# Kernel optimization log

Hardware: AMD Instinct MI355X
Metric: run time of the kernel (lower is better)

The kernel has to match this reference:

```python
import jax, jax.numpy as jnp
import numpy as np

NQ, NS, D, C = 4096, 16384, 128, 64  # queries, support, embed dim, num classes
T = 1.0
INF = 1000.0


def setup_inputs() -> dict:
    key = jax.random.key(0)
    k1, k2, k3 = jax.random.split(key, 3)
    xs = jax.random.normal(k1, (NS, D), dtype=jnp.float32)
    xq = jax.random.normal(k2, (NQ, D), dtype=jnp.float32)
    # labels 0..C-1, every class present with equal counts (NS/C = 256 > 1)
    ys = jax.random.permutation(k3, jnp.arange(NS, dtype=jnp.int32) % C)
    pos = jnp.arange(NQ, dtype=jnp.int32)   # queries are the first NQ support rows
    yq = ys[pos]
    return {"xq": xq, "yq": yq, "xs": xs, "ys": ys, "pos": pos}


def reference(xq, yq, xs, ys, pos):
    # classes = sorted unique labels; with labels in [0, C) and all present,
    # torch.unique(ys) == arange(C), so class index of label y is y itself.
    classes = jnp.arange(C, dtype=ys.dtype)
    one_hot = (ys[:, None] == classes[None, :]).astype(xq.dtype)   # [NS, C]
    counts = one_hot.sum(axis=0)                                   # [C]
    yq_new = ys[pos]                                               # class idx of each query
    idx = counts[yq] > 1                                           # queries with >1 same-class support

    # leave-one-out class prototypes per query
    mus = one_hot.T @ xs                                           # [C, D] per-class sums
    M = mus[yq_new] - xq                                           # [NQ, D]
    denom = jnp.clip(counts[yq_new] - 1.0, 0.1, None)              # [NQ]
    proto = M / denom[:, None]
    # pos_logit uses unsquared L2 distance (cdist p=2 .diag()) in the source
    pos_logit = -jnp.sqrt(jnp.maximum(jnp.sum((xq - proto) ** 2, axis=-1), 0.0))  # [NQ]

    # l2_dist logits: -0.5 * ||xq_i - xs_j||^2 / T, via the GEMM expansion
    sq = (jnp.sum(xq * xq, -1)[:, None] + jnp.sum(xs * xs, -1)[None, :]
          - 2.0 * (xq @ xs.T))                                     # [NQ, NS]
    logit = -0.5 * jnp.maximum(sq, 0.0) / T

    ind = jnp.arange(NQ)
    logit = logit.at[ind, pos].set(0.0)                            # logit[ind, pos] *= 0
    logit = logit.at[ind, pos].add(jnp.where(idx, -INF, 0.0))      # -= INF where idx

    # per-class masked segment sum == logit @ one_hot  -> [NQ, C]
    summed = logit @ one_hot
    normalized = summed / (counts - 1.0)[None, :]
    neg_logit = jax.scipy.special.logsumexp(normalized, axis=1)    # [NQ]
    return jnp.mean(neg_logit - pos_logit)
```

## Files before the change

### kernel.cpp

```cpp
#include <hip/hip_runtime.h>
#include <hip/hip_bf16.h>

#define NQ 4096
#define NS 16384
#define DIM 128
#define NC 64
#define INFV 1000.0f

using bf16 = __hip_bfloat16;
typedef __attribute__((ext_vector_type(8))) short frag_ab;
typedef __attribute__((ext_vector_type(4))) float frag_cd;

__device__ inline frag_ab pack8(float4 a, float4 b) {
    union { __hip_bfloat16 h; short s; } u;
    frag_ab f;
    u.h = __float2bfloat16(a.x); f[0] = u.s;
    u.h = __float2bfloat16(a.y); f[1] = u.s;
    u.h = __float2bfloat16(a.z); f[2] = u.s;
    u.h = __float2bfloat16(a.w); f[3] = u.s;
    u.h = __float2bfloat16(b.x); f[4] = u.s;
    u.h = __float2bfloat16(b.y); f[5] = u.s;
    u.h = __float2bfloat16(b.z); f[6] = u.s;
    u.h = __float2bfloat16(b.w); f[7] = u.s;
    return f;
}

__global__ __launch_bounds__(128) void k1_stats(
    const float* __restrict__ xs, const int* __restrict__ ys,
    float* __restrict__ mus_p, float* __restrict__ csum_p,
    int* __restrict__ counts_p) {
    const int c = blockIdx.x >> 1, half = blockIdx.x & 1;
    const int w = threadIdx.x >> 6, lane = threadIdx.x & 63;
    const int s = half * 2 + w;
    const int base = s * (NS / 4);
    const float2* xs2 = (const float2*)xs;

    float2 macc = {0.f, 0.f};
    float sacc = 0.f;
    int cnt = 0;
    for (int i = 0; i < NS / 4; i += 64) {
        int y = ys[base + i + lane];
        unsigned long long m = __ballot(y == c);
        cnt += (int)__popcll(m);
        while (m) {
            int b = __ffsll((long long)m) - 1;
            m &= m - 1;
            int row = base + i + b;
            float2 v = xs2[(size_t)row * 64 + lane];
            macc.x += v.x; macc.y += v.y;
            sacc += v.x * v.x + v.y * v.y;
        }
    }
    ((float2*)mus_p)[(size_t)(c * 4 + s) * 64 + lane] = macc;
#pragma unroll
    for (int mm = 1; mm < 64; mm <<= 1) sacc += __shfl_xor(sacc, mm, 64);
    if (lane == 0) {
        csum_p[c * 4 + s] = sacc;
        counts_p[c * 4 + s] = cnt;
    }
}

__global__ __launch_bounds__(256) void k2_main(
    const float* __restrict__ xq, const int* __restrict__ yq,
    const float* __restrict__ xs, const int* __restrict__ ys,
    const int* __restrict__ pos,
    const float* __restrict__ mus_p, const float* __restrict__ csum_p,
    const int* __restrict__ counts_p, float* __restrict__ out) {
    __shared__ float mus_lds[64 * 132];
    __shared__ float cnt_lds[64];
    __shared__ float csum_lds[64];
    __shared__ float sqq_a[64], corr_a[64], pospl_a[64];
    __shared__ int cp_a[64];
    __shared__ float red[4];

    const int tid = threadIdx.x, w = tid >> 6, lane = tid & 63;
    const int quad = lane >> 4, l15 = lane & 15;
    const int qbase = blockIdx.x * 64 + w * 16;

#pragma unroll 4
    for (int r = 0; r < 32; ++r) {
        int i = r * 256 + tid;
        int c = i >> 7, d = i & 127;
        float ssum = 0.f;
#pragma unroll
        for (int s = 0; s < 4; ++s) ssum += mus_p[(size_t)(c * 4 + s) * 128 + d];
        mus_lds[c * 132 + d] = ssum;
    }
    if (tid < 64) {
        float cs = 0.f; int cc = 0;
#pragma unroll
        for (int s = 0; s < 4; ++s) { cs += csum_p[tid * 4 + s]; cc += counts_p[tid * 4 + s]; }
        csum_lds[tid] = cs;
        cnt_lds[tid] = (float)cc;
    }
    __syncthreads();

    {
        int q_loc = lane >> 2, chunk = lane & 3;
        int q = qbase + q_loc;
        int pi = pos[q];
        int yqi = yq[q];
        int cp = ys[pi];
        float cnt_p = cnt_lds[cp];
        float inv_d = 1.f / fmaxf(cnt_p - 1.f, 0.1f);
        bool idxq = cnt_lds[yqi] > 1.f;
        float sqq = 0.f, dotv = 0.f, sqs = 0.f, dd = 0.f;
#pragma unroll
        for (int t = 0; t < 8; ++t) {
            int d0 = chunk * 32 + t * 4;
            float4 a = *(const float4*)(xq + (size_t)q * DIM + d0);
            float4 b = *(const float4*)(xs + (size_t)pi * DIM + d0);
            float4 m = *(const float4*)(&mus_lds[cp * 132 + d0]);
            sqq += a.x * a.x + a.y * a.y + a.z * a.z + a.w * a.w;
            dotv += a.x * b.x + a.y * b.y + a.z * b.z + a.w * b.w;
            sqs += b.x * b.x + b.y * b.y + b.z * b.z + b.w * b.w;
            float ex;
            ex = a.x - (m.x - a.x) * inv_d; dd += ex * ex;
            ex = a.y - (m.y - a.y) * inv_d; dd += ex * ex;
            ex = a.z - (m.z - a.z) * inv_d; dd += ex * ex;
            ex = a.w - (m.w - a.w) * inv_d; dd += ex * ex;
        }
#pragma unroll
        for (int mm = 1; mm < 4; mm <<= 1) {
            sqq += __shfl_xor(sqq, mm, 64);
            dotv += __shfl_xor(dotv, mm, 64);
            sqs += __shfl_xor(sqs, mm, 64);
            dd += __shfl_xor(dd, mm, 64);
        }
        if (chunk == 0) {
            float raw = -0.5f * fmaxf(sqq + sqs - 2.f * dotv, 0.f);
            sqq_a[w * 16 + q_loc] = sqq;
            corr_a[w * 16 + q_loc] = (idxq ? -INFV : 0.f) - raw;
            pospl_a[w * 16 + q_loc] = -sqrtf(fmaxf(dd, 0.f));
            cp_a[w * 16 + q_loc] = cp;
        }
    }
    __syncthreads();

    frag_ab afr[4];
    {
        const float* src0 = xq + (size_t)(qbase + l15) * DIM + quad * 8;
#pragma unroll
        for (int kk = 0; kk < 4; ++kk) {
            const float* s = src0 + kk * 32;
            afr[kk] = pack8(*(const float4*)s, *(const float4*)(s + 4));
        }
    }
    frag_cd acc[4];
#pragma unroll
    for (int ct = 0; ct < 4; ++ct) {
#pragma unroll
        for (int e = 0; e < 4; ++e) acc[ct][e] = 0.f;
        const float* bsrc = &mus_lds[(ct * 16 + l15) * 132 + quad * 8];
        frag_ab bfr[4];
#pragma unroll
        for (int kk = 0; kk < 4; ++kk) {
            const float* s = bsrc + kk * 32;
            bfr[kk] = pack8(*(const float4*)s, *(const float4*)(s + 4));
        }
#pragma unroll
        for (int kk = 0; kk < 4; ++kk)
            acc[ct] = __builtin_amdgcn_mfma_f32_16x16x32_bf16(afr[kk], bfr[kk], acc[ct], 0, 0, 0);
    }

    float norm[4][4];
#pragma unroll
    for (int ct = 0; ct < 4; ++ct) {
        int cB = ct * 16 + l15;
        float cc = cnt_lds[cB], cs = csum_lds[cB];
        float invc = 1.f / (cc - 1.f);
#pragma unroll
        for (int r = 0; r < 4; ++r) {
            int q_loc = quad * 4 + r;
            float sv = -0.5f * (cc * sqq_a[w * 16 + q_loc] + cs - 2.f * acc[ct][r]);
            if (cB == cp_a[w * 16 + q_loc]) sv += corr_a[w * 16 + q_loc];
            norm[ct][r] = sv * invc;
        }
    }
    float tacc = 0.f;
#pragma unroll
    for (int r = 0; r < 4; ++r) {
        float mx = fmaxf(fmaxf(norm[0][r], norm[1][r]), fmaxf(norm[2][r], norm[3][r]));
#pragma unroll
        for (int mm = 1; mm < 16; mm <<= 1) mx = fmaxf(mx, __shfl_xor(mx, mm, 64));
        float e = expf(norm[0][r] - mx) + expf(norm[1][r] - mx) +
                  expf(norm[2][r] - mx) + expf(norm[3][r] - mx);
#pragma unroll
        for (int mm = 1; mm < 16; mm <<= 1) e += __shfl_xor(e, mm, 64);
        float lse = mx + logf(e);
        tacc += lse - pospl_a[w * 16 + quad * 4 + r];
    }
    tacc = (l15 == 0) ? tacc : 0.f;
#pragma unroll
    for (int mm = 1; mm < 64; mm <<= 1) tacc += __shfl_xor(tacc, mm, 64);
    if (lane == 0) red[w] = tacc;
    __syncthreads();
    if (tid == 0)
        atomicAdd(out, (red[0] + red[1] + red[2] + red[3]) * (1.f / NQ));
}

extern "C" void kernel_launch(void* const* d_in, const int* in_sizes, int n_in,
                              void* d_out, int out_size, void* d_ws, size_t ws_size,
                              hipStream_t stream) {
    const float* xq = (const float*)d_in[0];
    const int* yq = (const int*)d_in[1];
    const float* xs = (const float*)d_in[2];
    const int* ys = (const int*)d_in[3];
    const int* pos = (const int*)d_in[4];
    float* out = (float*)d_out;

    char* wsp = (char*)d_ws;
    float* mus_p   = (float*)wsp; wsp += (size_t)NC * 4 * DIM * 4;
    float* csum_p  = (float*)wsp; wsp += NC * 4 * 4;
    int* counts_p  = (int*)wsp;   wsp += NC * 4 * 4;

    hipMemsetAsync(out, 0, sizeof(float), stream);
    k1_stats<<<NC * 2, 128, 0, stream>>>(xs, ys, mus_p, csum_p, counts_p);
    k2_main<<<NQ / 64, 256, 0, stream>>>(xq, yq, xs, ys, pos,
                                         mus_p, csum_p, counts_p, out);
}
```

Measured before the change: 113.6 us.

## Restructure class-stats kernel as LDS atomic histogram with slotted global reduction

The per-class statistics kernel now splits the support rows across 128 blocks instead of scanning all rows once per class. Each block accumulates class sums, squared norms and counts into shared memory with atomics, then atomically adds its partial into one of 8 global slots. The main kernel sums those 8 slots with vectorised loads. The output zeroing moves into the first kernel, a workspace memset replaces it, and exp/log switch to fast intrinsics. This removes the redundant per-class scan of ys and the low block count, at the cost of LDS and global atomic contention and an extra memset.

Result: slower. 121.5 us (+6.9%).

```diff
diff --git a/kernel.cpp b/kernel.cpp
--- a/kernel.cpp
+++ b/kernel.cpp
@@ -5,6 +5,7 @@
 #define NS 16384
 #define DIM 128
 #define NC 64
+#define NSLOT 8
 #define INFV 1000.0f
 
 using bf16 = __hip_bfloat16;
@@ -25,38 +26,47 @@
     return f;
 }
 
-__global__ __launch_bounds__(128) void k1_stats(
+__global__ __launch_bounds__(256) void k1_stats(
     const float* __restrict__ xs, const int* __restrict__ ys,
     float* __restrict__ mus_p, float* __restrict__ csum_p,
-    int* __restrict__ counts_p) {
-    const int c = blockIdx.x >> 1, half = blockIdx.x & 1;
-    const int w = threadIdx.x >> 6, lane = threadIdx.x & 63;
-    const int s = half * 2 + w;
-    const int base = s * (NS / 4);
+    float* __restrict__ cnt_p, float* __restrict__ out) {
+    __shared__ float hist[NC * DIM];
+    __shared__ float sq2[NC * 64];
+    __shared__ float ctl[NC];
+    const int tid = threadIdx.x, w = tid >> 6, lane = tid & 63;
+    for (int i = tid; i < NC * DIM; i += 256) hist[i] = 0.f;
+    for (int i = tid; i < NC * 64; i += 256) sq2[i] = 0.f;
+    if (tid < NC) ctl[tid] = 0.f;
+    if (blockIdx.x == 0 && tid == 0) out[0] = 0.f;
+    __syncthreads();
+
+    const int rbase = blockIdx.x * 128 + w * 32;
     const float2* xs2 = (const float2*)xs;
-
-    float2 macc = {0.f, 0.f};
-    float sacc = 0.f;
-    int cnt = 0;
-    for (int i = 0; i < NS / 4; i += 64) {
-        int y = ys[base + i + lane];
-        unsigned long long m = __ballot(y == c);
-        cnt += (int)__popcll(m);
-        while (m) {
-            int b = __ffsll((long long)m) - 1;
-            m &= m - 1;
-            int row = base + i + b;
-            float2 v = xs2[(size_t)row * 64 + lane];
-            macc.x += v.x; macc.y += v.y;
-            sacc += v.x * v.x + v.y * v.y;
-        }
-    }
-    ((float2*)mus_p)[(size_t)(c * 4 + s) * 64 + lane] = macc;
-#pragma unroll
-    for (int mm = 1; mm < 64; mm <<= 1) sacc += __shfl_xor(sacc, mm, 64);
-    if (lane == 0) {
-        csum_p[c * 4 + s] = sacc;
-        counts_p[c * 4 + s] = cnt;
+#pragma unroll 4
+    for (int i = 0; i < 32; ++i) {
+        int r = rbase + i;
+        int cls = ys[r];
+        float2 v = xs2[(size_t)r * 64 + lane];
+        atomicAdd(&hist[cls * DIM + lane * 2], v.x);
+        atomicAdd(&hist[cls * DIM + lane * 2 + 1], v.y);
+        atomicAdd(&sq2[cls * 64 + lane], v.x * v.x + v.y * v.y);
+        if (lane == 0) atomicAdd(&ctl[cls], 1.f);
+    }
+    __syncthreads();
+
+    const int slot = blockIdx.x & (NSLOT - 1);
+    float* mslot = mus_p + (size_t)slot * NC * DIM;
+    const int rot = (blockIdx.x * 1031) & (NC * DIM - 1);
+    for (int i = tid; i < NC * DIM; i += 256) {
+        int j = (i + rot) & (NC * DIM - 1);
+        atomicAdd(&mslot[j], hist[j]);
+    }
+    if (tid < NC) {
+        float s = 0.f;
+#pragma unroll
+        for (int l = 0; l < 64; ++l) s += sq2[tid * 64 + l];
+        atomicAdd(&csum_p[slot * NC + tid], s);
+        atomicAdd(&cnt_p[slot * NC + tid], ctl[tid]);
     }
 }
 
@@ -65,7 +75,7 @@
     const float* __restrict__ xs, const int* __restrict__ ys,
     const int* __restrict__ pos,
     const float* __restrict__ mus_p, const float* __restrict__ csum_p,
-    const int* __restrict__ counts_p, float* __restrict__ out) {
+    const float* __restrict__ cnt_p, float* __restrict__ out) {
     __shared__ float mus_lds[64 * 132];
     __shared__ float cnt_lds[64];
     __shared__ float csum_lds[64];
@@ -77,21 +87,33 @@
     const int quad = lane >> 4, l15 = lane & 15;
     const int qbase = blockIdx.x * 64 + w * 16;
 
-#pragma unroll 4
-    for (int r = 0; r < 32; ++r) {
-        int i = r * 256 + tid;
-        int c = i >> 7, d = i & 127;
-        float ssum = 0.f;
-#pragma unroll
-        for (int s = 0; s < 4; ++s) ssum += mus_p[(size_t)(c * 4 + s) * 128 + d];
-        mus_lds[c * 132 + d] = ssum;
-    }
-    if (tid < 64) {
-        float cs = 0.f; int cc = 0;
-#pragma unroll
-        for (int s = 0; s < 4; ++s) { cs += csum_p[tid * 4 + s]; cc += counts_p[tid * 4 + s]; }
-        csum_lds[tid] = cs;
-        cnt_lds[tid] = (float)cc;
+    {
+        int c = tid >> 2, d0 = (tid & 3) * 32;
+        float4 a4[8];
+#pragma unroll
+        for (int t = 0; t < 8; ++t) a4[t] = make_float4(0.f, 0.f, 0.f, 0.f);
+#pragma unroll
+        for (int sl = 0; sl < NSLOT; ++sl) {
+            const float* src = mus_p + (size_t)sl * NC * DIM + c * DIM + d0;
+#pragma unroll
+            for (int t = 0; t < 8; ++t) {
+                float4 v = *(const float4*)(src + t * 4);
+                a4[t].x += v.x; a4[t].y += v.y; a4[t].z += v.z; a4[t].w += v.w;
+            }
+        }
+#pragma unroll
+        for (int t = 0; t < 8; ++t)
+            *(float4*)(&mus_lds[c * 132 + d0 + t * 4]) = a4[t];
+        if (tid < NC) {
+            float cs = 0.f, cc = 0.f;
+#pragma unroll
+            for (int sl = 0; sl < NSLOT; ++sl) {
+                cs += csum_p[sl * NC + tid];
+                cc += cnt_p[sl * NC + tid];
+            }
+            csum_lds[tid] = cs;
+            cnt_lds[tid] = cc;
+        }
     }
     __syncthreads();
 
@@ -101,8 +123,8 @@
         int pi = pos[q];
         int yqi = yq[q];
         int cp = ys[pi];
-        float cnt_p = cnt_lds[cp];
-        float inv_d = 1.f / fmaxf(cnt_p - 1.f, 0.1f);
+        float cnt_pv = cnt_lds[cp];
+        float inv_d = 1.f / fmaxf(cnt_pv - 1.f, 0.1f);
         bool idxq = cnt_lds[yqi] > 1.f;
         float sqq = 0.f, dotv = 0.f, sqs = 0.f, dd = 0.f;
 #pragma unroll
@@ -183,11 +205,11 @@
         float mx = fmaxf(fmaxf(norm[0][r], norm[1][r]), fmaxf(norm[2][r], norm[3][r]));
 #pragma unroll
         for (int mm = 1; mm < 16; mm <<= 1) mx = fmaxf(mx, __shfl_xor(mx, mm, 64));
-        float e = expf(norm[0][r] - mx) + expf(norm[1][r] - mx) +
-                  expf(norm[2][r] - mx) + expf(norm[3][r] - mx);
+        float e = __expf(norm[0][r] - mx) + __expf(norm[1][r] - mx) +
+                  __expf(norm[2][r] - mx) + __expf(norm[3][r] - mx);
 #pragma unroll
         for (int mm = 1; mm < 16; mm <<= 1) e += __shfl_xor(e, mm, 64);
-        float lse = mx + logf(e);
+        float lse = mx + __logf(e);
         tacc += lse - pospl_a[w * 16 + quad * 4 + r];
     }
     tacc = (l15 == 0) ? tacc : 0.f;
@@ -210,12 +232,13 @@
     float* out = (float*)d_out;
 
     char* wsp = (char*)d_ws;
-    float* mus_p   = (float*)wsp; wsp += (size_t)NC * 4 * DIM * 4;
-    float* csum_p  = (float*)wsp; wsp += NC * 4 * 4;
-    int* counts_p  = (int*)wsp;   wsp += NC * 4 * 4;
-
-    hipMemsetAsync(out, 0, sizeof(float), stream);
-    k1_stats<<<NC * 2, 128, 0, stream>>>(xs, ys, mus_p, csum_p, counts_p);
+    float* mus_p  = (float*)wsp; wsp += (size_t)NSLOT * NC * DIM * 4;
+    float* csum_p = (float*)wsp; wsp += NSLOT * NC * 4;
+    float* cnt_p  = (float*)wsp; wsp += NSLOT * NC * 4;
+    size_t zbytes = (size_t)NSLOT * NC * DIM * 4 + 2 * (size_t)NSLOT * NC * 4;
+
+    hipMemsetAsync(d_ws, 0, zbytes, stream);
+    k1_stats<<<NS / 128, 256, 0, stream>>>(xs, ys, mus_p, csum_p, cnt_p, out);
     k2_main<<<NQ / 64, 256, 0, stream>>>(xq, yq, xs, ys, pos,
-                                         mus_p, csum_p, counts_p, out);
-}
+                                         mus_p, csum_p, cnt_p, out);
+}
```
